# Optimization experiments

Hardware: AMD Instinct MI355X
Metric: run time of the kernel (lower is better)

## Reference

```python
import jax, jax.numpy as jnp
import numpy as np

EMB = 1024
HEADS = 16
HEAD_DIM = EMB // HEADS
FF = 4 * EMB
EPS = 1e-5


def gelu_tanh(x):
    c = jnp.sqrt(jnp.asarray(2.0 / jnp.pi, dtype=x.dtype))
    return 0.5 * x * (1.0 + jnp.tanh(c * (x + 0.044715 * x ** 3)))


def layernorm(x, scale, bias):
    mean = jnp.mean(x, axis=-1, keepdims=True)
    # torch x.var() default is unbiased (ddof=1)
    var = jnp.var(x, axis=-1, keepdims=True, ddof=1)
    return (x - mean) / jnp.sqrt(var + EPS) * scale + bias


def setup_inputs() -> dict:
    key = jax.random.key(0)
    ks = jax.random.split(key, 12)
    s = lambda k, shape, sc=0.02: (jax.random.normal(k, shape, dtype=jnp.float32) * sc)
    return {
        "x": jax.random.normal(ks[0], (4, 2048, EMB), dtype=jnp.float32),
        "Wq": s(ks[1], (EMB, EMB)),
        "Wk": s(ks[2], (EMB, EMB)),
        "Wv": s(ks[3], (EMB, EMB)),
        "Wo": s(ks[4], (EMB, EMB)),
        "bo": jnp.zeros((EMB,), jnp.float32),
        "ln1_scale": jnp.ones((EMB,), jnp.float32),
        "ln1_bias": jnp.zeros((EMB,), jnp.float32),
        "ln2_scale": jnp.ones((EMB,), jnp.float32),
        "ln2_bias": jnp.zeros((EMB,), jnp.float32),
        "W1": s(ks[5], (EMB, FF)),
        "b1": jnp.zeros((FF,), jnp.float32),
        "W2": s(ks[6], (FF, EMB)),
        "b2": jnp.zeros((EMB,), jnp.float32),
    }


def reference(x, Wq, Wk, Wv, Wo, bo, ln1_scale, ln1_bias, ln2_scale, ln2_bias, W1, b1, W2, b2):
    b, n, _ = x.shape
    # --- attention sub-block (pre-LN) ---
    h = layernorm(x, ln1_scale, ln1_bias)
    q = (h @ Wq).reshape(b, n, HEADS, HEAD_DIM).transpose(0, 2, 1, 3)  # b,h,s,d
    k = (h @ Wk).reshape(b, n, HEADS, HEAD_DIM).transpose(0, 2, 1, 3)
    v = (h @ Wv).reshape(b, n, HEADS, HEAD_DIM).transpose(0, 2, 1, 3)
    scores = jnp.einsum("bhqd,bhkd->bhqk", q, k)
    causal = jnp.tril(jnp.ones((n, n), dtype=bool))
    scores = jnp.where(causal, scores, -jnp.inf)
    attn = jax.nn.softmax(scores / jnp.sqrt(jnp.asarray(HEAD_DIM, scores.dtype)), axis=-1)
    ctx = jnp.einsum("bhqk,bhkd->bhqd", attn, v).transpose(0, 2, 1, 3).reshape(b, n, EMB)
    attn_out = ctx @ Wo + bo
    x = x + attn_out  # dropout = identity (eval)
    # --- MLP sub-block ---
    h = layernorm(x, ln2_scale, ln2_bias)
    h = gelu_tanh(h @ W1 + b1) @ W2 + b2
    return x + h
```

## Files before the change

### kernel.cpp

```cpp
#include <hip/hip_runtime.h>
#include <hip/hip_bf16.h>
#include <math.h>

typedef __hip_bfloat16 bf16;
typedef __attribute__((ext_vector_type(8))) short short8;
typedef __attribute__((ext_vector_type(4))) float floatx4;

#define EMB   1024
#define SEQ   2048
#define BATCH 4
#define M_TOK 8192
#define HEADS 16
#define HDIM  64
#define FFDIM 4096
#define KVB   64

typedef __attribute__((address_space(3))) void lds_t;
typedef __attribute__((address_space(1))) void glob_t;

static __device__ __forceinline__ void gll16(const bf16* g, bf16* l) {
  __builtin_amdgcn_global_load_lds((const glob_t*)g, (lds_t*)l, 16, 0, 0);
}

static __device__ __forceinline__ unsigned short f2bu(float f) {
  union { __hip_bfloat16 h; unsigned short u; } cv;
  cv.h = __float2bfloat16(f);
  return cv.u;
}

static __device__ __forceinline__ float gelu_f(float x) {
  float t = tanhf(0.7978845608028654f * (x + 0.044715f * x * x * x));
  return 0.5f * x * (1.0f + t);
}

__global__ __launch_bounds__(256) void wconv_kernel(const float* __restrict__ W,
                                                    bf16* __restrict__ Wt,
                                                    int Kd, int Nd) {
  __shared__ float tile[32][33];
  int n0 = blockIdx.x * 32, k0 = blockIdx.y * 32;
  int tx = threadIdx.x & 31, ty = threadIdx.x >> 5;
  #pragma unroll
  for (int j = 0; j < 32; j += 8)
    tile[ty + j][tx] = W[(size_t)(k0 + ty + j) * Nd + n0 + tx];
  __syncthreads();
  #pragma unroll
  for (int j = 0; j < 32; j += 8)
    Wt[(size_t)(n0 + ty + j) * Kd + k0 + tx] = __float2bfloat16(tile[tx][ty + j]);
}

__global__ __launch_bounds__(256) void ln_kernel(const float* __restrict__ x,
                                                 const float* __restrict__ sc,
                                                 const float* __restrict__ bi,
                                                 bf16* __restrict__ out) {
  int row = blockIdx.x, tid = threadIdx.x;
  const float4* xr = (const float4*)(x + (size_t)row * EMB);
  float4 v = xr[tid];
  float s  = v.x + v.y + v.z + v.w;
  float s2 = v.x * v.x + v.y * v.y + v.z * v.z + v.w * v.w;
  #pragma unroll
  for (int off = 1; off < 64; off <<= 1) {
    s  += __shfl_xor(s, off);
    s2 += __shfl_xor(s2, off);
  }
  __shared__ float red[8];
  int wv = tid >> 6;
  if ((tid & 63) == 0) { red[wv] = s; red[4 + wv] = s2; }
  __syncthreads();
  s  = red[0] + red[1] + red[2] + red[3];
  s2 = red[4] + red[5] + red[6] + red[7];
  float mean = s * (1.0f / EMB);
  float var  = (s2 - (float)EMB * mean * mean) * (1.0f / (EMB - 1));
  float rstd = rsqrtf(var + 1e-5f);
  float4 scv = ((const float4*)sc)[tid];
  float4 biv = ((const float4*)bi)[tid];
  ushort4 o;
  o.x = f2bu((v.x - mean) * rstd * scv.x + biv.x);
  o.y = f2bu((v.y - mean) * rstd * scv.y + biv.y);
  o.z = f2bu((v.z - mean) * rstd * scv.z + biv.z);
  o.w = f2bu((v.w - mean) * rstd * scv.w + biv.w);
  ((ushort4*)(out + (size_t)row * EMB))[tid] = o;
}

template<int Nd, int Kd, int MODE>
__global__ __launch_bounds__(256, 2) void gemm_kernel(
    const bf16* __restrict__ A, const bf16* __restrict__ Bt,
    const float* __restrict__ bias, const float* __restrict__ resid,
    void* __restrict__ outp) {
  __shared__ __align__(16) bf16 As[128 * 32];
  __shared__ __align__(16) bf16 Bs[128 * 32];
  const int m0 = blockIdx.x * 128, n0 = blockIdx.y * 128;
  const int tid = threadIdx.x;
  const int lane = tid & 63, wave = tid >> 6;
  const int lo = lane & 15, hi = lane >> 4;
  const int wr = wave >> 1, wc = wave & 1;

  const bf16* Bt2 = Bt;
  if constexpr (MODE == 6) Bt2 = Bt + ((size_t)blockIdx.z << 20);

  floatx4 acc[4][4];
  #pragma unroll
  for (int i = 0; i < 4; i++)
    #pragma unroll
    for (int j = 0; j < 4; j++)
      #pragma unroll
      for (int r = 0; r < 4; r++) acc[i][j][r] = 0.0f;

  const bf16* Ab = A   + (size_t)m0 * Kd;
  const bf16* Bb = Bt2 + (size_t)n0 * Kd;

  for (int k0 = 0; k0 < Kd; k0 += 32) {
    #pragma unroll
    for (int s = 0; s < 2; ++s) {
      int c = tid + s * 256;
      gll16(Ab + (size_t)(c >> 2) * Kd + k0 + (c & 3) * 8, As + c * 8);
      gll16(Bb + (size_t)(c >> 2) * Kd + k0 + (c & 3) * 8, Bs + c * 8);
    }
    __syncthreads();
    short8 af[4], bfr[4];
    #pragma unroll
    for (int i = 0; i < 4; i++)
      af[i] = *(const short8*)&As[(wr * 64 + i * 16 + lo) * 32 + hi * 8];
    #pragma unroll
    for (int j = 0; j < 4; j++)
      bfr[j] = *(const short8*)&Bs[(wc * 64 + j * 16 + lo) * 32 + hi * 8];
    #pragma unroll
    for (int i = 0; i < 4; i++)
      #pragma unroll
      for (int j = 0; j < 4; j++)
        acc[i][j] = __builtin_amdgcn_mfma_f32_16x16x32_bf16(af[i], bfr[j], acc[i][j], 0, 0, 0);
    __syncthreads();
  }

  #pragma unroll
  for (int i = 0; i < 4; i++) {
    #pragma unroll
    for (int j = 0; j < 4; j++) {
      const int mb = m0 + wr * 64 + i * 16 + hi * 4;
      const int n  = n0 + wc * 64 + j * 16 + lo;
      if constexpr (MODE == 6) {
        const int z = blockIdx.z;
        const int bb = mb >> 11, hhh = n >> 6, d = n & 63;
        bf16* ob = (bf16*)outp + ((size_t)z << 23);
        if (z == 2) {
          ushort4 pk;
          pk.x = f2bu(acc[i][j][0]); pk.y = f2bu(acc[i][j][1]);
          pk.z = f2bu(acc[i][j][2]); pk.w = f2bu(acc[i][j][3]);
          *(ushort4*)&ob[((size_t)(bb * HEADS + hhh) * HDIM + d) * SEQ + (mb & 2047)] = pk;
        } else {
          const float sc = (z == 0) ? 0.125f : 1.0f;
          #pragma unroll
          for (int r = 0; r < 4; r++) {
            const int ss = (mb + r) & 2047;
            ob[((size_t)(bb * HEADS + hhh) * SEQ + ss) * HDIM + d] =
                __float2bfloat16(acc[i][j][r] * sc);
          }
        }
      } else if constexpr (MODE == 3 || MODE == 5) {
        #pragma unroll
        for (int r = 0; r < 4; r++) {
          const int m = mb + r;
          ((float*)outp)[(size_t)m * EMB + n] =
              acc[i][j][r] + bias[n] + resid[(size_t)m * EMB + n];
        }
      } else if constexpr (MODE == 4) {
        #pragma unroll
        for (int r = 0; r < 4; r++)
          ((bf16*)outp)[(size_t)(mb + r) * FFDIM + n] =
              __float2bfloat16(gelu_f(acc[i][j][r] + bias[n]));
      }
    }
  }
}

__global__ __launch_bounds__(256, 2) void attn_kernel(
    const bf16* __restrict__ q, const bf16* __restrict__ k,
    const bf16* __restrict__ vt, bf16* __restrict__ ctx) {
  __shared__ __align__(16) char KVs[2][2][64 * 128];
  __shared__ __align__(16) char Pls[4][4096];
  const int bh = blockIdx.x, qt = blockIdx.y;
  const int tid = threadIdx.x;
  const int wave = tid >> 6, lane = tid & 63;
  const int lo = lane & 15, hi = lane >> 4;
  const int lo7 = lo & 7;
  const int q0 = qt * 128;
  const int q0w = q0 + wave * 32;
  const int qmax = q0w + 31;

  const bf16* qp = q  + ((size_t)bh * SEQ + q0w) * HDIM;
  const bf16* kp = k  + (size_t)bh * SEQ * HDIM;
  const bf16* vp = vt + (size_t)bh * HDIM * SEQ;

  short8 qf[2][2];
  #pragma unroll
  for (int m = 0; m < 2; m++)
    #pragma unroll
    for (int kk = 0; kk < 2; kk++)
      qf[m][kk] = *(const short8*)&qp[(size_t)(m * 16 + lo) * HDIM + kk * 32 + hi * 8];

  float m_run[2] = {-1e30f, -1e30f};
  float l_run[2] = {0.0f, 0.0f};
  floatx4 o[4][2];
  #pragma unroll
  for (int df = 0; df < 4; df++)
    #pragma unroll
    for (int m = 0; m < 2; m++)
      #pragma unroll
      for (int r = 0; r < 4; r++) o[df][m][r] = 0.0f;

  const int nt = 2 * qt + 2;

  const int c0 = tid, c1 = tid + 256;
  const int r0 = c0 >> 3, s0 = (c0 & 7) ^ (r0 & 7);
  const int r1 = c1 >> 3, s1 = (c1 & 7) ^ (r1 & 7);

  gll16(kp + (size_t)r0 * HDIM + s0 * 8, (bf16*)&KVs[0][0][c0 * 16]);
  gll16(vp + (size_t)r0 * SEQ + s0 * 8,  (bf16*)&KVs[0][1][c0 * 16]);
  gll16(kp + (size_t)r1 * HDIM + s1 * 8, (bf16*)&KVs[0][0][c1 * 16]);
  gll16(vp + (size_t)r1 * SEQ + s1 * 8,  (bf16*)&KVs[0][1][c1 * 16]);

  for (int t = 0; t < nt; ++t) {
    const int buf = t & 1;
    const int k0 = t * KVB;
    if (t + 1 < nt) {
      const int kn = k0 + KVB;
      gll16(kp + (size_t)(kn + r0) * HDIM + s0 * 8, (bf16*)&KVs[buf ^ 1][0][c0 * 16]);
      gll16(vp + (size_t)r0 * SEQ + kn + s0 * 8,    (bf16*)&KVs[buf ^ 1][1][c0 * 16]);
      gll16(kp + (size_t)(kn + r1) * HDIM + s1 * 8, (bf16*)&KVs[buf ^ 1][0][c1 * 16]);
      gll16(vp + (size_t)r1 * SEQ + kn + s1 * 8,    (bf16*)&KVs[buf ^ 1][1][c1 * 16]);
      asm volatile("s_waitcnt vmcnt(4)" ::: "memory");
    } else {
      asm volatile("s_waitcnt vmcnt(0)" ::: "memory");
    }
    __builtin_amdgcn_s_barrier();
    __builtin_amdgcn_sched_barrier(0);

    if (k0 <= qmax) {
      const char* Kb = KVs[buf][0];
      const char* Vb = KVs[buf][1];
      floatx4 sfr[4][2];
      #pragma unroll
      for (int kf = 0; kf < 4; kf++) {
        const int rowb = (kf * 16 + lo) * 128;
        short8 kf0 = *(const short8*)(Kb + rowb + (( 0 + hi * 16) ^ (lo7 << 4)));
        short8 kf1 = *(const short8*)(Kb + rowb + ((64 + hi * 16) ^ (lo7 << 4)));
        #pragma unroll
        for (int m = 0; m < 2; m++) {
          floatx4 z = {0.0f, 0.0f, 0.0f, 0.0f};
          z = __builtin_amdgcn_mfma_f32_16x16x32_bf16(kf0, qf[m][0], z, 0, 0, 0);
          z = __builtin_amdgcn_mfma_f32_16x16x32_bf16(kf1, qf[m][1], z, 0, 0, 0);
          sfr[kf][m] = z;
        }
      }
      if (k0 + KVB - 1 > q0w) {
        #pragma unroll
        for (int m = 0; m < 2; m++) {
          const int qg = q0w + m * 16 + lo;
          #pragma unroll
          for (int kf = 0; kf < 4; kf++)
            #pragma unroll
            for (int r = 0; r < 4; r++) {
              const int key = k0 + kf * 16 + hi * 4 + r;
              if (key > qg) sfr[kf][m][r] = -1e30f;
            }
        }
      }
      float alpha[2];
      #pragma unroll
      for (int m = 0; m < 2; m++) {
        float tmax = -1e30f;
        #pragma unroll
        for (int kf = 0; kf < 4; kf++)
          #pragma unroll
          for (int r = 0; r < 4; r++) tmax = fmaxf(tmax, sfr[kf][m][r]);
        tmax = fmaxf(tmax, __shfl_xor(tmax, 16));
        tmax = fmaxf(tmax, __shfl_xor(tmax, 32));
        const float mn = fmaxf(m_run[m], tmax);
        alpha[m] = __expf(m_run[m] - mn);
        m_run[m] = mn;
        float ps = 0.0f;
        const int prow = (m * 16 + lo) * 128;
        #pragma unroll
        for (int kf = 0; kf < 4; kf++) {
          float p0 = __expf(sfr[kf][m][0] - mn);
          float p1 = __expf(sfr[kf][m][1] - mn);
          float p2 = __expf(sfr[kf][m][2] - mn);
          float p3 = __expf(sfr[kf][m][3] - mn);
          ps += (p0 + p1) + (p2 + p3);
          ushort4 pk;
          pk.x = f2bu(p0); pk.y = f2bu(p1); pk.z = f2bu(p2); pk.w = f2bu(p3);
          *(ushort4*)(Pls[wave] + prow + ((kf * 32 + hi * 8) ^ (lo7 << 4))) = pk;
        }
        ps += __shfl_xor(ps, 16);
        ps += __shfl_xor(ps, 32);
        l_run[m] = l_run[m] * alpha[m] + ps;
      }
      asm volatile("s_waitcnt lgkmcnt(0)" ::: "memory");
      __builtin_amdgcn_sched_barrier(0);
      short8 pa[2][2];
      #pragma unroll
      for (int m = 0; m < 2; m++)
        #pragma unroll
        for (int kk2 = 0; kk2 < 2; kk2++)
          pa[m][kk2] = *(const short8*)(Pls[wave] + (m * 16 + lo) * 128 +
                                        ((kk2 * 64 + hi * 16) ^ (lo7 << 4)));
      float ar[2][4];
      #pragma unroll
      for (int m = 0; m < 2; m++)
        #pragma unroll
        for (int r = 0; r < 4; r++) ar[m][r] = __shfl(alpha[m], hi * 4 + r);
      #pragma unroll
      for (int df = 0; df < 4; df++)
        #pragma unroll
        for (int m = 0; m < 2; m++)
          #pragma unroll
          for (int r = 0; r < 4; r++) o[df][m][r] *= ar[m][r];
      #pragma unroll
      for (int df = 0; df < 4; df++) {
        const int rowb = (df * 16 + lo) * 128;
        short8 vf0 = *(const short8*)(Vb + rowb + (( 0 + hi * 16) ^ (lo7 << 4)));
        short8 vf1 = *(const short8*)(Vb + rowb + ((64 + hi * 16) ^ (lo7 << 4)));
        #pragma unroll
        for (int m = 0; m < 2; m++) {
          o[df][m] = __builtin_amdgcn_mfma_f32_16x16x32_bf16(pa[m][0], vf0, o[df][m], 0, 0, 0);
          o[df][m] = __builtin_amdgcn_mfma_f32_16x16x32_bf16(pa[m][1], vf1, o[df][m], 0, 0, 0);
        }
      }
    }
    __builtin_amdgcn_s_barrier();
    __builtin_amdgcn_sched_barrier(0);
  }

  const int b = bh >> 4, hh = bh & 15;
  #pragma unroll
  for (int m = 0; m < 2; m++) {
    float lr[4];
    #pragma unroll
    for (int r = 0; r < 4; r++) lr[r] = __shfl(l_run[m], hi * 4 + r);
    #pragma unroll
    for (int df = 0; df < 4; df++)
      #pragma unroll
      for (int r = 0; r < 4; r++) {
        const int srow = q0w + m * 16 + hi * 4 + r;
        ctx[((size_t)(b * SEQ + srow)) * EMB + hh * HDIM + df * 16 + lo] =
            __float2bfloat16(o[df][m][r] / lr[r]);
      }
  }
}

extern "C" void kernel_launch(void* const* d_in, const int* in_sizes, int n_in,
                              void* d_out, int out_size, void* d_ws, size_t ws_size,
                              hipStream_t stream) {
  const float* x   = (const float*)d_in[0];
  const float* Wq  = (const float*)d_in[1];
  const float* Wk  = (const float*)d_in[2];
  const float* Wv  = (const float*)d_in[3];
  const float* Wo  = (const float*)d_in[4];
  const float* bo  = (const float*)d_in[5];
  const float* l1s = (const float*)d_in[6];
  const float* l1b = (const float*)d_in[7];
  const float* l2s = (const float*)d_in[8];
  const float* l2b = (const float*)d_in[9];
  const float* W1  = (const float*)d_in[10];
  const float* b1  = (const float*)d_in[11];
  const float* W2  = (const float*)d_in[12];
  const float* b2  = (const float*)d_in[13];
  float* out = (float*)d_out;

  char* ws = (char*)d_ws;
  bf16* hbuf   = (bf16*)(ws);
  bf16* qbuf   = (bf16*)(ws + ((size_t)16 << 20));
  bf16* kbuf   = (bf16*)(ws + ((size_t)32 << 20));
  bf16* vbuf   = (bf16*)(ws + ((size_t)48 << 20));
  bf16* ctxbuf = hbuf;
  bf16* gbuf   = (bf16*)(ws);
  bf16* h2buf  = (bf16*)(ws + ((size_t)64 << 20));
  bf16* WqT    = (bf16*)(ws + ((size_t)80 << 20));
  bf16* WkT    = WqT + (1u << 20);
  bf16* WvT    = WkT + (1u << 20);
  bf16* WoT    = WvT + (1u << 20);
  bf16* W1T    = WoT + (1u << 20);
  bf16* W2T    = W1T + (4u << 20);

  wconv_kernel<<<dim3(32, 32), 256, 0, stream>>>(Wq, WqT, 1024, 1024);
  wconv_kernel<<<dim3(32, 32), 256, 0, stream>>>(Wk, WkT, 1024, 1024);
  wconv_kernel<<<dim3(32, 32), 256, 0, stream>>>(Wv, WvT, 1024, 1024);
  wconv_kernel<<<dim3(32, 32), 256, 0, stream>>>(Wo, WoT, 1024, 1024);
  wconv_kernel<<<dim3(128, 32), 256, 0, stream>>>(W1, W1T, 1024, 4096);
  wconv_kernel<<<dim3(32, 128), 256, 0, stream>>>(W2, W2T, 4096, 1024);

  ln_kernel<<<8192, 256, 0, stream>>>(x, l1s, l1b, hbuf);

  gemm_kernel<1024, 1024, 6><<<dim3(64, 8, 3), 256, 0, stream>>>(hbuf, WqT, nullptr, nullptr, qbuf);

  attn_kernel<<<dim3(64, 16), 256, 0, stream>>>(qbuf, kbuf, vbuf, ctxbuf);

  gemm_kernel<1024, 1024, 3><<<dim3(64, 8), 256, 0, stream>>>(ctxbuf, WoT, bo, x, (void*)out);
  ln_kernel<<<8192, 256, 0, stream>>>(out, l2s, l2b, h2buf);
  gemm_kernel<4096, 1024, 4><<<dim3(64, 32), 256, 0, stream>>>(h2buf, W1T, b1, nullptr, gbuf);
  gemm_kernel<1024, 4096, 5><<<dim3(64, 8), 256, 0, stream>>>(gbuf, W2T, b2, out, (void*)out);
}
```

Measured before the change: 521.9 us.

## Replace GEMMs with 256-row double-buffered 8-wave kernel and raise MFMA priority

The GEMM kernel moves from 128x128 tiles with BK=32 and four waves to 256xBN tiles with BK=64 and eight waves. The LDS tiles are double-buffered with an XOR-swizzled layout, and the next tile is prefetched while the current one is computed. MFMA sections in both the GEMM and the attention kernel are wrapped in s_setprio. The intent is to improve data reuse, hide global-load latency, cut LDS bank conflicts and keep the matrix cores busy. In exchange it runs one block per CU with heavier register and LDS use, adds more barriers per K step, and launches fewer blocks.

```diff
diff --git a/kernel.cpp b/kernel.cpp
--- a/kernel.cpp
+++ b/kernel.cpp
@@ -20,6 +20,13 @@
 
 static __device__ __forceinline__ void gll16(const bf16* g, bf16* l) {
   __builtin_amdgcn_global_load_lds((const glob_t*)g, (lds_t*)l, 16, 0, 0);
+}
+
+template<int N>
+static __device__ __forceinline__ void wait_vmcnt() {
+  if constexpr (N == 0) asm volatile("s_waitcnt vmcnt(0)" ::: "memory");
+  else if constexpr (N == 6) asm volatile("s_waitcnt vmcnt(6)" ::: "memory");
+  else if constexpr (N == 8) asm volatile("s_waitcnt vmcnt(8)" ::: "memory");
 }
 
 static __device__ __forceinline__ unsigned short f2bu(float f) {
@@ -81,81 +88,129 @@
   ((ushort4*)(out + (size_t)row * EMB))[tid] = o;
 }
 
-template<int Nd, int Kd, int MODE>
-__global__ __launch_bounds__(256, 2) void gemm_kernel(
+template<int BN, int WMv, int WNv, int Kd, int MODE>
+__global__ __launch_bounds__(512, 1) void gemm8_kernel(
     const bf16* __restrict__ A, const bf16* __restrict__ Bt,
     const float* __restrict__ bias, const float* __restrict__ resid,
     void* __restrict__ outp) {
-  __shared__ __align__(16) bf16 As[128 * 32];
-  __shared__ __align__(16) bf16 Bs[128 * 32];
-  const int m0 = blockIdx.x * 128, n0 = blockIdx.y * 128;
+  constexpr int BM = 256, BK = 64;
+  constexpr int MR = BM / WMv / 16;
+  constexpr int NR = BN / WNv / 16;
+  constexpr int HR = MR / 2;
+  constexpr int ACH = (BM * BK) / 8 / 512;
+  constexpr int BCH = (BN * BK) / 8 / 512;
+  constexpr int NLD = ACH + BCH;
+  constexpr int NT = Kd / BK;
+
+  __shared__ __align__(16) bf16 As[2][BM * BK];
+  __shared__ __align__(16) bf16 Bs[2][BN * BK];
+
   const int tid = threadIdx.x;
   const int lane = tid & 63, wave = tid >> 6;
-  const int lo = lane & 15, hi = lane >> 4;
-  const int wr = wave >> 1, wc = wave & 1;
+  const int lo = lane & 15, hi = lane >> 4, lo7 = lane & 7;
+  const int wm = wave / WNv, wn = wave % WNv;
+  const int m0 = blockIdx.x * BM, n0 = blockIdx.y * BN;
 
   const bf16* Bt2 = Bt;
   if constexpr (MODE == 6) Bt2 = Bt + ((size_t)blockIdx.z << 20);
-
-  floatx4 acc[4][4];
-  #pragma unroll
-  for (int i = 0; i < 4; i++)
-    #pragma unroll
-    for (int j = 0; j < 4; j++)
+  const bf16* Ag = A + (size_t)m0 * Kd;
+  const bf16* Bg = Bt2 + (size_t)n0 * Kd;
+
+  auto STAGE = [&](int kt, int bufb) {
+    const int k0 = kt * BK;
+    #pragma unroll
+    for (int i = 0; i < ACH; i++) {
+      const int ch = i * 512 + tid;
+      const int r = ch >> 3, s = (ch & 7) ^ (r & 7);
+      gll16(Ag + (size_t)r * Kd + k0 + s * 8, (bf16*)As[bufb] + ch * 8);
+    }
+    #pragma unroll
+    for (int i = 0; i < BCH; i++) {
+      const int ch = i * 512 + tid;
+      const int r = ch >> 3, s = (ch & 7) ^ (r & 7);
+      gll16(Bg + (size_t)r * Kd + k0 + s * 8, (bf16*)Bs[bufb] + ch * 8);
+    }
+  };
+
+  floatx4 acc[MR][NR];
+  #pragma unroll
+  for (int i = 0; i < MR; i++)
+    #pragma unroll
+    for (int j = 0; j < NR; j++)
       #pragma unroll
       for (int r = 0; r < 4; r++) acc[i][j][r] = 0.0f;
 
-  const bf16* Ab = A   + (size_t)m0 * Kd;
-  const bf16* Bb = Bt2 + (size_t)n0 * Kd;
-
-  for (int k0 = 0; k0 < Kd; k0 += 32) {
-    #pragma unroll
-    for (int s = 0; s < 2; ++s) {
-      int c = tid + s * 256;
-      gll16(Ab + (size_t)(c >> 2) * Kd + k0 + (c & 3) * 8, As + c * 8);
-      gll16(Bb + (size_t)(c >> 2) * Kd + k0 + (c & 3) * 8, Bs + c * 8);
-    }
-    __syncthreads();
-    short8 af[4], bfr[4];
-    #pragma unroll
-    for (int i = 0; i < 4; i++)
-      af[i] = *(const short8*)&As[(wr * 64 + i * 16 + lo) * 32 + hi * 8];
-    #pragma unroll
-    for (int j = 0; j < 4; j++)
-      bfr[j] = *(const short8*)&Bs[(wc * 64 + j * 16 + lo) * 32 + hi * 8];
-    #pragma unroll
-    for (int i = 0; i < 4; i++)
-      #pragma unroll
-      for (int j = 0; j < 4; j++)
-        acc[i][j] = __builtin_amdgcn_mfma_f32_16x16x32_bf16(af[i], bfr[j], acc[i][j], 0, 0, 0);
-    __syncthreads();
+  STAGE(0, 0);
+
+  for (int t = 0; t < NT; ++t) {
+    const int bb = t & 1;
+    const bf16* Ab = As[bb];
+    const bf16* Bb = Bs[bb];
+    short8 bfr[NR];
+    #pragma unroll
+    for (int p = 0; p < 4; p++) {
+      const int kk = p >> 1, mh = p & 1;
+      if (p == 0) {
+        if (t + 1 < NT) { STAGE(t + 1, bb ^ 1); wait_vmcnt<NLD>(); }
+        else            { wait_vmcnt<0>(); }
+        __builtin_amdgcn_s_barrier();
+        __builtin_amdgcn_sched_barrier(0);
+      }
+      short8 af[HR];
+      #pragma unroll
+      for (int i = 0; i < HR; i++) {
+        const int r = wm * (MR * 16) + (mh * HR + i) * 16 + lo;
+        af[i] = *(const short8*)&Ab[r * 64 + ((kk * 4 + hi) ^ lo7) * 8];
+      }
+      if (mh == 0) {
+        #pragma unroll
+        for (int n = 0; n < NR; n++) {
+          const int r = wn * (NR * 16) + n * 16 + lo;
+          bfr[n] = *(const short8*)&Bb[r * 64 + ((kk * 4 + hi) ^ lo7) * 8];
+        }
+      }
+      if (p > 0) __builtin_amdgcn_s_barrier();
+      asm volatile("s_waitcnt lgkmcnt(0)" ::: "memory");
+      __builtin_amdgcn_sched_barrier(0);
+      __builtin_amdgcn_s_setprio(1);
+      #pragma unroll
+      for (int i = 0; i < HR; i++)
+        #pragma unroll
+        for (int n = 0; n < NR; n++)
+          acc[mh * HR + i][n] =
+              __builtin_amdgcn_mfma_f32_16x16x32_bf16(af[i], bfr[n], acc[mh * HR + i][n], 0, 0, 0);
+      __builtin_amdgcn_s_setprio(0);
+      __builtin_amdgcn_s_barrier();
+    }
   }
 
-  #pragma unroll
-  for (int i = 0; i < 4; i++) {
-    #pragma unroll
-    for (int j = 0; j < 4; j++) {
-      const int mb = m0 + wr * 64 + i * 16 + hi * 4;
-      const int n  = n0 + wc * 64 + j * 16 + lo;
+  const int mwb = m0 + wm * (MR * 16);
+  const int nwb = n0 + wn * (NR * 16);
+  #pragma unroll
+  for (int i = 0; i < MR; i++) {
+    #pragma unroll
+    for (int j = 0; j < NR; j++) {
+      const int mb = mwb + i * 16 + hi * 4;
+      const int n  = nwb + j * 16 + lo;
       if constexpr (MODE == 6) {
         const int z = blockIdx.z;
-        const int bb = mb >> 11, hhh = n >> 6, d = n & 63;
+        const int bx = mb >> 11, hhh = n >> 6, d = n & 63;
         bf16* ob = (bf16*)outp + ((size_t)z << 23);
         if (z == 2) {
           ushort4 pk;
           pk.x = f2bu(acc[i][j][0]); pk.y = f2bu(acc[i][j][1]);
           pk.z = f2bu(acc[i][j][2]); pk.w = f2bu(acc[i][j][3]);
-          *(ushort4*)&ob[((size_t)(bb * HEADS + hhh) * HDIM + d) * SEQ + (mb & 2047)] = pk;
+          *(ushort4*)&ob[((size_t)(bx * HEADS + hhh) * HDIM + d) * SEQ + (mb & 2047)] = pk;
         } else {
           const float sc = (z == 0) ? 0.125f : 1.0f;
           #pragma unroll
           for (int r = 0; r < 4; r++) {
             const int ss = (mb + r) & 2047;
-            ob[((size_t)(bb * HEADS + hhh) * SEQ + ss) * HDIM + d] =
+            ob[((size_t)(bx * HEADS + hhh) * SEQ + ss) * HDIM + d] =
                 __float2bfloat16(acc[i][j][r] * sc);
           }
         }
-      } else if constexpr (MODE == 3 || MODE == 5) {
+      } else if constexpr (MODE == 3) {
         #pragma unroll
         for (int r = 0; r < 4; r++) {
           const int m = mb + r;
@@ -238,6 +293,7 @@
       const char* Kb = KVs[buf][0];
       const char* Vb = KVs[buf][1];
       floatx4 sfr[4][2];
+      __builtin_amdgcn_s_setprio(1);
       #pragma unroll
       for (int kf = 0; kf < 4; kf++) {
         const int rowb = (kf * 16 + lo) * 128;
@@ -251,6 +307,7 @@
           sfr[kf][m] = z;
         }
       }
+      __builtin_amdgcn_s_setprio(0);
       if (k0 + KVB - 1 > q0w) {
         #pragma unroll
         for (int m = 0; m < 2; m++) {
@@ -314,6 +371,7 @@
         for (int m = 0; m < 2; m++)
           #pragma unroll
           for (int r = 0; r < 4; r++) o[df][m][r] *= ar[m][r];
+      __builtin_amdgcn_s_setprio(1);
       #pragma unroll
       for (int df = 0; df < 4; df++) {
         const int rowb = (df * 16 + lo) * 128;
@@ -325,6 +383,7 @@
           o[df][m] = __builtin_amdgcn_mfma_f32_16x16x32_bf16(pa[m][1], vf1, o[df][m], 0, 0, 0);
         }
       }
+      __builtin_amdgcn_s_setprio(0);
     }
     __builtin_amdgcn_s_barrier();
     __builtin_amdgcn_sched_barrier(0);
@@ -390,12 +449,16 @@
 
   ln_kernel<<<8192, 256, 0, stream>>>(x, l1s, l1b, hbuf);
 
-  gemm_kernel<1024, 1024, 6><<<dim3(64, 8, 3), 256, 0, stream>>>(hbuf, WqT, nullptr, nullptr, qbuf);
+  gemm8_kernel<128, 4, 2, 1024, 6><<<dim3(32, 8, 3), 512, 0, stream>>>(
+      hbuf, WqT, nullptr, nullptr, qbuf);
 
   attn_kernel<<<dim3(64, 16), 256, 0, stream>>>(qbuf, kbuf, vbuf, ctxbuf);
 
-  gemm_kernel<1024, 1024, 3><<<dim3(64, 8), 256, 0, stream>>>(ctxbuf, WoT, bo, x, (void*)out);
+  gemm8_kernel<128, 4, 2, 1024, 3><<<dim3(32, 8), 512, 0, stream>>>(
+      ctxbuf, WoT, bo, x, (void*)out);
   ln_kernel<<<8192, 256, 0, stream>>>(out, l2s, l2b, h2buf);
-  gemm_kernel<4096, 1024, 4><<<dim3(64, 32), 256, 0, stream>>>(h2buf, W1T, b1, nullptr, gbuf);
-  gemm_kernel<1024, 4096, 5><<<dim3(64, 8), 256, 0, stream>>>(gbuf, W2T, b2, out, (void*)out);
-}
+  gemm8_kernel<256, 2, 4, 1024, 4><<<dim3(32, 16), 512, 0, stream>>>(
+      h2buf, W1T, b1, nullptr, gbuf);
+  gemm8_kernel<128, 4, 2, 4096, 3><<<dim3(32, 8), 512, 0, stream>>>(
+      gbuf, W2T, b2, out, (void*)out);
+}
```

New measurement: 560.0 us. +7.3%, slower.

## Replace GEMM with 256-row 8-wave double-buffered ping-pong pipelined kernel

Applied to the files above, without the earlier changes.

Replaces the 128x128, single-stage GEMM with a 512-thread kernel using 256xBN tiles, BK=64 and double-buffered LDS. Global-to-LDS loads for the next k-tile are interleaved with MFMA quarter-tiles, and an XOR swizzle avoids LDS bank conflicts. MFMA sections get raised wave priority via s_setprio, in both the GEMM and the attention kernel. The QKV projection now runs as one N=3072 GEMM instead of using the z dimension. Larger tiles raise register and LDS use and leave fewer blocks for the smaller GEMMs.

```diff
diff --git a/kernel.cpp b/kernel.cpp
--- a/kernel.cpp
+++ b/kernel.cpp
@@ -81,92 +81,158 @@
   ((ushort4*)(out + (size_t)row * EMB))[tid] = o;
 }
 
-template<int Nd, int Kd, int MODE>
-__global__ __launch_bounds__(256, 2) void gemm_kernel(
+template<int BN, int Kd, int MODE>
+__global__ __launch_bounds__(512, 1) void gemm8_kernel(
     const bf16* __restrict__ A, const bf16* __restrict__ Bt,
     const float* __restrict__ bias, const float* __restrict__ resid,
     void* __restrict__ outp) {
-  __shared__ __align__(16) bf16 As[128 * 32];
-  __shared__ __align__(16) bf16 Bs[128 * 32];
-  const int m0 = blockIdx.x * 128, n0 = blockIdx.y * 128;
+  constexpr int BM = 256, BK = 64;
+  constexpr int MR = 8, MRh = 4;
+  constexpr int NR = BN / 64, NRh = NR / 2;
+  constexpr int BLOADS = BN / 128;
+  constexpr int NT = Kd / BK;
+
+  __shared__ __align__(16) bf16 As[2][2][128 * 64];
+  __shared__ __align__(16) bf16 Bs[2][2][(BN / 2) * 64];
+
   const int tid = threadIdx.x;
   const int lane = tid & 63, wave = tid >> 6;
-  const int lo = lane & 15, hi = lane >> 4;
-  const int wr = wave >> 1, wc = wave & 1;
-
-  const bf16* Bt2 = Bt;
-  if constexpr (MODE == 6) Bt2 = Bt + ((size_t)blockIdx.z << 20);
-
-  floatx4 acc[4][4];
-  #pragma unroll
-  for (int i = 0; i < 4; i++)
-    #pragma unroll
-    for (int j = 0; j < 4; j++)
+  const int lo = lane & 15, hi = lane >> 4, lo7 = lane & 7;
+  const int wm = wave >> 2, wn = wave & 3;
+  const int m0 = blockIdx.x * BM, n0 = blockIdx.y * BN;
+
+  const bf16* Ag = A  + (size_t)m0 * Kd;
+  const bf16* Bg = Bt + (size_t)n0 * Kd;
+
+  auto SA = [&](int h, int b, int kt) {
+    #pragma unroll
+    for (int l = 0; l < 2; l++) {
+      const int ch = l * 512 + tid;
+      const int r = (ch >> 3) & 63;
+      const int row = ((ch >> 9) << 7) + h * 64 + r;
+      const int slot = (ch & 7) ^ (r & 7);
+      gll16(Ag + (size_t)row * Kd + kt * BK + slot * 8, &As[b][h][0] + ch * 8);
+    }
+  };
+  auto SB = [&](int h, int b, int kt) {
+    #pragma unroll
+    for (int l = 0; l < BLOADS; l++) {
+      const int ch = l * 512 + tid;
+      int row, r;
+      if constexpr (BN == 256) { r = (ch >> 3) & 31; row = ((ch >> 8) << 6) + h * 32 + r; }
+      else                     { r = (ch >> 3) & 15; row = ((ch >> 7) << 5) + h * 16 + r; }
+      const int slot = (ch & 7) ^ (r & 7);
+      gll16(Bg + (size_t)row * Kd + kt * BK + slot * 8, &Bs[b][h][0] + ch * 8);
+    }
+  };
+
+  auto RA = [&](int h, int b, short8 (&af)[MRh][2]) {
+    #pragma unroll
+    for (int i = 0; i < MRh; i++)
+      #pragma unroll
+      for (int kk = 0; kk < 2; kk++)
+        af[i][kk] = *(const short8*)&As[b][h][(wm * 64 + i * 16 + lo) * 64 +
+                                             (((kk * 4 + hi) ^ lo7) * 8)];
+  };
+  auto RB = [&](int h, int b, short8 (&bf)[NRh][2]) {
+    #pragma unroll
+    for (int j = 0; j < NRh; j++)
+      #pragma unroll
+      for (int kk = 0; kk < 2; kk++)
+        bf[j][kk] = *(const short8*)&Bs[b][h][(wn * (BN / 8) + j * 16 + lo) * 64 +
+                                              (((kk * 4 + hi) ^ lo7) * 8)];
+  };
+
+  floatx4 acc[MR][NR];
+  #pragma unroll
+  for (int i = 0; i < MR; i++)
+    #pragma unroll
+    for (int j = 0; j < NR; j++)
       #pragma unroll
       for (int r = 0; r < 4; r++) acc[i][j][r] = 0.0f;
 
-  const bf16* Ab = A   + (size_t)m0 * Kd;
-  const bf16* Bb = Bt2 + (size_t)n0 * Kd;
-
-  for (int k0 = 0; k0 < Kd; k0 += 32) {
-    #pragma unroll
-    for (int s = 0; s < 2; ++s) {
-      int c = tid + s * 256;
-      gll16(Ab + (size_t)(c >> 2) * Kd + k0 + (c & 3) * 8, As + c * 8);
-      gll16(Bb + (size_t)(c >> 2) * Kd + k0 + (c & 3) * 8, Bs + c * 8);
-    }
-    __syncthreads();
-    short8 af[4], bfr[4];
-    #pragma unroll
-    for (int i = 0; i < 4; i++)
-      af[i] = *(const short8*)&As[(wr * 64 + i * 16 + lo) * 32 + hi * 8];
-    #pragma unroll
-    for (int j = 0; j < 4; j++)
-      bfr[j] = *(const short8*)&Bs[(wc * 64 + j * 16 + lo) * 32 + hi * 8];
-    #pragma unroll
-    for (int i = 0; i < 4; i++)
-      #pragma unroll
-      for (int j = 0; j < 4; j++)
-        acc[i][j] = __builtin_amdgcn_mfma_f32_16x16x32_bf16(af[i], bfr[j], acc[i][j], 0, 0, 0);
-    __syncthreads();
+  short8 af[MRh][2], bf0[NRh][2], bf1[NRh][2];
+
+  auto MM = [&](int mh, int nh, short8 (&a)[MRh][2], short8 (&bb)[NRh][2]) {
+    __builtin_amdgcn_s_setprio(1);
+    #pragma unroll
+    for (int kk = 0; kk < 2; kk++)
+      #pragma unroll
+      for (int i = 0; i < MRh; i++)
+        #pragma unroll
+        for (int j = 0; j < NRh; j++)
+          acc[mh * MRh + i][nh * NRh + j] = __builtin_amdgcn_mfma_f32_16x16x32_bf16(
+              a[i][kk], bb[j][kk], acc[mh * MRh + i][nh * NRh + j], 0, 0, 0);
+    __builtin_amdgcn_s_setprio(0);
+  };
+  auto BAR = [&]() {
+    __builtin_amdgcn_s_barrier();
+    __builtin_amdgcn_sched_barrier(0);
+  };
+
+  SA(0, 0, 0); SB(0, 0, 0); SA(1, 0, 0); SB(1, 0, 0);
+
+  for (int t = 0; t < NT; ++t) {
+    const int b = t & 1, bn = b ^ 1;
+    const bool L = (t + 1 == NT);
+    if (!L) { SA(0, bn, t + 1); asm volatile("s_waitcnt vmcnt(2)" ::: "memory"); }
+    else    { asm volatile("s_waitcnt vmcnt(0)" ::: "memory"); }
+    BAR();
+    RA(0, b, af); RB(0, b, bf0);
+    MM(0, 0, af, bf0);
+    BAR();
+    RB(1, b, bf1);
+    if (!L) SB(0, bn, t + 1);
+    BAR();
+    MM(0, 1, af, bf1);
+    BAR();
+    RA(1, b, af);
+    if (!L) SA(1, bn, t + 1);
+    BAR();
+    MM(1, 1, af, bf1);
+    BAR();
+    if (!L) SB(1, bn, t + 1);
+    BAR();
+    MM(1, 0, af, bf0);
+    BAR();
   }
 
   #pragma unroll
-  for (int i = 0; i < 4; i++) {
-    #pragma unroll
-    for (int j = 0; j < 4; j++) {
-      const int mb = m0 + wr * 64 + i * 16 + hi * 4;
-      const int n  = n0 + wc * 64 + j * 16 + lo;
+  for (int ri = 0; ri < MR; ri++) {
+    const int mb = m0 + wm * 128 + (ri >> 2) * 64 + (ri & 3) * 16 + hi * 4;
+    #pragma unroll
+    for (int cj = 0; cj < NR; cj++) {
+      const int n = n0 + wn * (BN / 4) + (cj / NRh) * (BN / 8) + (cj % NRh) * 16 + lo;
       if constexpr (MODE == 6) {
-        const int z = blockIdx.z;
-        const int bb = mb >> 11, hhh = n >> 6, d = n & 63;
+        const int z = n >> 10, nz = n & 1023;
+        const int bx = mb >> 11, hhh = nz >> 6, d = nz & 63;
         bf16* ob = (bf16*)outp + ((size_t)z << 23);
         if (z == 2) {
           ushort4 pk;
-          pk.x = f2bu(acc[i][j][0]); pk.y = f2bu(acc[i][j][1]);
-          pk.z = f2bu(acc[i][j][2]); pk.w = f2bu(acc[i][j][3]);
-          *(ushort4*)&ob[((size_t)(bb * HEADS + hhh) * HDIM + d) * SEQ + (mb & 2047)] = pk;
+          pk.x = f2bu(acc[ri][cj][0]); pk.y = f2bu(acc[ri][cj][1]);
+          pk.z = f2bu(acc[ri][cj][2]); pk.w = f2bu(acc[ri][cj][3]);
+          *(ushort4*)&ob[((size_t)(bx * HEADS + hhh) * HDIM + d) * SEQ + (mb & 2047)] = pk;
         } else {
           const float sc = (z == 0) ? 0.125f : 1.0f;
           #pragma unroll
           for (int r = 0; r < 4; r++) {
             const int ss = (mb + r) & 2047;
-            ob[((size_t)(bb * HEADS + hhh) * SEQ + ss) * HDIM + d] =
-                __float2bfloat16(acc[i][j][r] * sc);
+            ob[((size_t)(bx * HEADS + hhh) * SEQ + ss) * HDIM + d] =
+                __float2bfloat16(acc[ri][cj][r] * sc);
           }
         }
-      } else if constexpr (MODE == 3 || MODE == 5) {
+      } else if constexpr (MODE == 3) {
         #pragma unroll
         for (int r = 0; r < 4; r++) {
           const int m = mb + r;
           ((float*)outp)[(size_t)m * EMB + n] =
-              acc[i][j][r] + bias[n] + resid[(size_t)m * EMB + n];
+              acc[ri][cj][r] + bias[n] + resid[(size_t)m * EMB + n];
         }
       } else if constexpr (MODE == 4) {
         #pragma unroll
         for (int r = 0; r < 4; r++)
           ((bf16*)outp)[(size_t)(mb + r) * FFDIM + n] =
-              __float2bfloat16(gelu_f(acc[i][j][r] + bias[n]));
+              __float2bfloat16(gelu_f(acc[ri][cj][r] + bias[n]));
       }
     }
   }
@@ -238,6 +304,7 @@
       const char* Kb = KVs[buf][0];
       const char* Vb = KVs[buf][1];
       floatx4 sfr[4][2];
+      __builtin_amdgcn_s_setprio(1);
       #pragma unroll
       for (int kf = 0; kf < 4; kf++) {
         const int rowb = (kf * 16 + lo) * 128;
@@ -251,6 +318,7 @@
           sfr[kf][m] = z;
         }
       }
+      __builtin_amdgcn_s_setprio(0);
       if (k0 + KVB - 1 > q0w) {
         #pragma unroll
         for (int m = 0; m < 2; m++) {
@@ -314,6 +382,7 @@
         for (int m = 0; m < 2; m++)
           #pragma unroll
           for (int r = 0; r < 4; r++) o[df][m][r] *= ar[m][r];
+      __builtin_amdgcn_s_setprio(1);
       #pragma unroll
       for (int df = 0; df < 4; df++) {
         const int rowb = (df * 16 + lo) * 128;
@@ -325,6 +394,7 @@
           o[df][m] = __builtin_amdgcn_mfma_f32_16x16x32_bf16(pa[m][1], vf1, o[df][m], 0, 0, 0);
         }
       }
+      __builtin_amdgcn_s_setprio(0);
     }
     __builtin_amdgcn_s_barrier();
     __builtin_amdgcn_sched_barrier(0);
@@ -390,12 +460,16 @@
 
   ln_kernel<<<8192, 256, 0, stream>>>(x, l1s, l1b, hbuf);
 
-  gemm_kernel<1024, 1024, 6><<<dim3(64, 8, 3), 256, 0, stream>>>(hbuf, WqT, nullptr, nullptr, qbuf);
+  gemm8_kernel<256, 1024, 6><<<dim3(32, 12), 512, 0, stream>>>(
+      hbuf, WqT, nullptr, nullptr, qbuf);
 
   attn_kernel<<<dim3(64, 16), 256, 0, stream>>>(qbuf, kbuf, vbuf, ctxbuf);
 
-  gemm_kernel<1024, 1024, 3><<<dim3(64, 8), 256, 0, stream>>>(ctxbuf, WoT, bo, x, (void*)out);
+  gemm8_kernel<128, 1024, 3><<<dim3(32, 8), 512, 0, stream>>>(
+      ctxbuf, WoT, bo, x, (void*)out);
   ln_kernel<<<8192, 256, 0, stream>>>(out, l2s, l2b, h2buf);
-  gemm_kernel<4096, 1024, 4><<<dim3(64, 32), 256, 0, stream>>>(h2buf, W1T, b1, nullptr, gbuf);
-  gemm_kernel<1024, 4096, 5><<<dim3(64, 8), 256, 0, stream>>>(gbuf, W2T, b2, out, (void*)out);
-}
+  gemm8_kernel<256, 1024, 4><<<dim3(32, 16), 512, 0, stream>>>(
+      h2buf, W1T, b1, nullptr, gbuf);
+  gemm8_kernel<128, 4096, 3><<<dim3(32, 8), 512, 0, stream>>>(
+      gbuf, W2T, b2, out, (void*)out);
+}
```

New measurement: 545.1 us. +4.4%, slower.

## Double-buffer GEMM LDS tiles with async prefetch, XOR swizzle, and MFMA priority

Applied to the files above, without the earlier changes.

Rewrites the GEMM main loop to use two LDS buffers. The next K-tile is prefetched with global_load_lds while MFMAs run on the current tile, replacing two full __syncthreads per iteration with one barrier plus a vmcnt wait. It also adds an XOR swizzle of the 16-byte slots to cut LDS bank conflicts, raises launch bounds to 4 blocks per SM, and wraps the MFMA sections in s_setprio in both the GEMM and attention kernels. The doubled LDS use and the higher occupancy hint may force register spilling.

```diff
diff --git a/kernel.cpp b/kernel.cpp
--- a/kernel.cpp
+++ b/kernel.cpp
@@ -81,54 +81,74 @@
   ((ushort4*)(out + (size_t)row * EMB))[tid] = o;
 }
 
-template<int Nd, int Kd, int MODE>
-__global__ __launch_bounds__(256, 2) void gemm_kernel(
+template<int Kd, int MODE>
+__global__ __launch_bounds__(256, 4) void gemm2_kernel(
     const bf16* __restrict__ A, const bf16* __restrict__ Bt,
     const float* __restrict__ bias, const float* __restrict__ resid,
     void* __restrict__ outp) {
-  __shared__ __align__(16) bf16 As[128 * 32];
-  __shared__ __align__(16) bf16 Bs[128 * 32];
-  const int m0 = blockIdx.x * 128, n0 = blockIdx.y * 128;
+  constexpr int NT = Kd / 32;
+  __shared__ __align__(16) bf16 As[2][128 * 32];
+  __shared__ __align__(16) bf16 Bs[2][128 * 32];
   const int tid = threadIdx.x;
   const int lane = tid & 63, wave = tid >> 6;
   const int lo = lane & 15, hi = lane >> 4;
   const int wr = wave >> 1, wc = wave & 1;
+  const int m0 = blockIdx.x * 128, n0 = blockIdx.y * 128;
 
   const bf16* Bt2 = Bt;
   if constexpr (MODE == 6) Bt2 = Bt + ((size_t)blockIdx.z << 20);
-
-  floatx4 acc[4][4];
-  #pragma unroll
-  for (int i = 0; i < 4; i++)
-    #pragma unroll
-    for (int j = 0; j < 4; j++)
-      #pragma unroll
-      for (int r = 0; r < 4; r++) acc[i][j][r] = 0.0f;
-
   const bf16* Ab = A   + (size_t)m0 * Kd;
   const bf16* Bb = Bt2 + (size_t)n0 * Kd;
 
-  for (int k0 = 0; k0 < Kd; k0 += 32) {
+  auto STAGE = [&](int t, int b) {
     #pragma unroll
     for (int s = 0; s < 2; ++s) {
-      int c = tid + s * 256;
-      gll16(Ab + (size_t)(c >> 2) * Kd + k0 + (c & 3) * 8, As + c * 8);
-      gll16(Bb + (size_t)(c >> 2) * Kd + k0 + (c & 3) * 8, Bs + c * 8);
-    }
-    __syncthreads();
+      const int c = tid + s * 256;
+      const int row = c >> 2, slot = (c & 3) ^ (row & 3);
+      gll16(Ab + (size_t)row * Kd + t * 32 + slot * 8, As[b] + c * 8);
+      gll16(Bb + (size_t)row * Kd + t * 32 + slot * 8, Bs[b] + c * 8);
+    }
+  };
+
+  floatx4 acc[4][4];
+  #pragma unroll
+  for (int i = 0; i < 4; i++)
+    #pragma unroll
+    for (int j = 0; j < 4; j++)
+      #pragma unroll
+      for (int r = 0; r < 4; r++) acc[i][j][r] = 0.0f;
+
+  STAGE(0, 0);
+
+  for (int t = 0; t < NT; ++t) {
+    const int bb = t & 1;
+    __builtin_amdgcn_s_barrier();
+    __builtin_amdgcn_sched_barrier(0);
+    if (t + 1 < NT) {
+      STAGE(t + 1, bb ^ 1);
+      asm volatile("s_waitcnt vmcnt(4)" ::: "memory");
+    } else {
+      asm volatile("s_waitcnt vmcnt(0)" ::: "memory");
+    }
+    __builtin_amdgcn_sched_barrier(0);
     short8 af[4], bfr[4];
     #pragma unroll
-    for (int i = 0; i < 4; i++)
-      af[i] = *(const short8*)&As[(wr * 64 + i * 16 + lo) * 32 + hi * 8];
-    #pragma unroll
-    for (int j = 0; j < 4; j++)
-      bfr[j] = *(const short8*)&Bs[(wc * 64 + j * 16 + lo) * 32 + hi * 8];
+    for (int i = 0; i < 4; i++) {
+      const int row = wr * 64 + i * 16 + lo;
+      af[i] = *(const short8*)&As[bb][row * 32 + ((hi ^ (lo & 3)) * 8)];
+    }
+    #pragma unroll
+    for (int j = 0; j < 4; j++) {
+      const int row = wc * 64 + j * 16 + lo;
+      bfr[j] = *(const short8*)&Bs[bb][row * 32 + ((hi ^ (lo & 3)) * 8)];
+    }
+    __builtin_amdgcn_s_setprio(1);
     #pragma unroll
     for (int i = 0; i < 4; i++)
       #pragma unroll
       for (int j = 0; j < 4; j++)
         acc[i][j] = __builtin_amdgcn_mfma_f32_16x16x32_bf16(af[i], bfr[j], acc[i][j], 0, 0, 0);
-    __syncthreads();
+    __builtin_amdgcn_s_setprio(0);
   }
 
   #pragma unroll
@@ -139,23 +159,23 @@
       const int n  = n0 + wc * 64 + j * 16 + lo;
       if constexpr (MODE == 6) {
         const int z = blockIdx.z;
-        const int bb = mb >> 11, hhh = n >> 6, d = n & 63;
+        const int bx = mb >> 11, hhh = n >> 6, d = n & 63;
         bf16* ob = (bf16*)outp + ((size_t)z << 23);
         if (z == 2) {
           ushort4 pk;
           pk.x = f2bu(acc[i][j][0]); pk.y = f2bu(acc[i][j][1]);
           pk.z = f2bu(acc[i][j][2]); pk.w = f2bu(acc[i][j][3]);
-          *(ushort4*)&ob[((size_t)(bb * HEADS + hhh) * HDIM + d) * SEQ + (mb & 2047)] = pk;
+          *(ushort4*)&ob[((size_t)(bx * HEADS + hhh) * HDIM + d) * SEQ + (mb & 2047)] = pk;
         } else {
           const float sc = (z == 0) ? 0.125f : 1.0f;
           #pragma unroll
           for (int r = 0; r < 4; r++) {
             const int ss = (mb + r) & 2047;
-            ob[((size_t)(bb * HEADS + hhh) * SEQ + ss) * HDIM + d] =
+            ob[((size_t)(bx * HEADS + hhh) * SEQ + ss) * HDIM + d] =
                 __float2bfloat16(acc[i][j][r] * sc);
           }
         }
-      } else if constexpr (MODE == 3 || MODE == 5) {
+      } else if constexpr (MODE == 3) {
         #pragma unroll
         for (int r = 0; r < 4; r++) {
           const int m = mb + r;
@@ -238,6 +258,7 @@
       const char* Kb = KVs[buf][0];
       const char* Vb = KVs[buf][1];
       floatx4 sfr[4][2];
+      __builtin_amdgcn_s_setprio(1);
       #pragma unroll
       for (int kf = 0; kf < 4; kf++) {
         const int rowb = (kf * 16 + lo) * 128;
@@ -251,6 +272,7 @@
           sfr[kf][m] = z;
         }
       }
+      __builtin_amdgcn_s_setprio(0);
       if (k0 + KVB - 1 > q0w) {
         #pragma unroll
         for (int m = 0; m < 2; m++) {
@@ -314,6 +336,7 @@
         for (int m = 0; m < 2; m++)
           #pragma unroll
           for (int r = 0; r < 4; r++) o[df][m][r] *= ar[m][r];
+      __builtin_amdgcn_s_setprio(1);
       #pragma unroll
       for (int df = 0; df < 4; df++) {
         const int rowb = (df * 16 + lo) * 128;
@@ -325,6 +348,7 @@
           o[df][m] = __builtin_amdgcn_mfma_f32_16x16x32_bf16(pa[m][1], vf1, o[df][m], 0, 0, 0);
         }
       }
+      __builtin_amdgcn_s_setprio(0);
     }
     __builtin_amdgcn_s_barrier();
     __builtin_amdgcn_sched_barrier(0);
@@ -390,12 +414,16 @@
 
   ln_kernel<<<8192, 256, 0, stream>>>(x, l1s, l1b, hbuf);
 
-  gemm_kernel<1024, 1024, 6><<<dim3(64, 8, 3), 256, 0, stream>>>(hbuf, WqT, nullptr, nullptr, qbuf);
+  gemm2_kernel<1024, 6><<<dim3(64, 8, 3), 256, 0, stream>>>(
+      hbuf, WqT, nullptr, nullptr, qbuf);
 
   attn_kernel<<<dim3(64, 16), 256, 0, stream>>>(qbuf, kbuf, vbuf, ctxbuf);
 
-  gemm_kernel<1024, 1024, 3><<<dim3(64, 8), 256, 0, stream>>>(ctxbuf, WoT, bo, x, (void*)out);
+  gemm2_kernel<1024, 3><<<dim3(64, 8), 256, 0, stream>>>(
+      ctxbuf, WoT, bo, x, (void*)out);
   ln_kernel<<<8192, 256, 0, stream>>>(out, l2s, l2b, h2buf);
-  gemm_kernel<4096, 1024, 4><<<dim3(64, 32), 256, 0, stream>>>(h2buf, W1T, b1, nullptr, gbuf);
-  gemm_kernel<1024, 4096, 5><<<dim3(64, 8), 256, 0, stream>>>(gbuf, W2T, b2, out, (void*)out);
-}
+  gemm2_kernel<1024, 4><<<dim3(64, 32), 256, 0, stream>>>(
+      h2buf, W1T, b1, nullptr, gbuf);
+  gemm2_kernel<4096, 3><<<dim3(64, 8), 256, 0, stream>>>(
+      gbuf, W2T, b2, out, (void*)out);
+}
```

Result: no change. 519.1 us (-0.5%).
